# Kernel optimization log

Measured on AMD Instinct MI355X. Metric: run time of the kernel, lower is better.

The kernel has to match this reference:

```python
import jax, jax.numpy as jnp
import numpy as np

MIN_MAP = jnp.array([-3.602826, -3.602826, -3.602826], dtype=jnp.float32)

def _conv(x, w, stride, pad):
    return jax.lax.conv_general_dilated(x, w, (stride, stride), [(pad, pad), (pad, pad)],
                                        dimension_numbers=('NCHW', 'OIHW', 'NCHW'))

def _bn(x, g, b):
    # inference BatchNorm with running_mean=0, running_var=1 -> pure channel affine
    return x * g[None, :, None, None] + b[None, :, None, None]

def _maxpool2(x):
    return jax.lax.reduce_window(x, -jnp.inf, jax.lax.max, (1, 1, 2, 2), (1, 1, 2, 2), 'VALID')

def _rotations(angles):
    # angles: [N,3] (already multiplied by pi); matrix entries copied verbatim from the torch source
    c, s = jnp.cos(angles), jnp.sin(angles)
    z = jnp.zeros_like(c[:, 0]); o = jnp.ones_like(c[:, 0])
    Rx = jnp.stack([jnp.stack([o, z, z], -1),
                    jnp.stack([z, c[:, 0], s[:, 0]], -1),
                    jnp.stack([z, -s[:, 0], c[:, 0]], -1)], 1)
    Ry = jnp.stack([jnp.stack([c[:, 1], z, -s[:, 1]], -1),
                    jnp.stack([z, o, z], -1),
                    jnp.stack([s[:, 1], z, c[:, 1]], -1)], 1)
    Rz = jnp.stack([jnp.stack([c[:, 2], s[:, 2], z], -1),
                    jnp.stack([-s[:, 2], c[:, 2], z], -1),
                    jnp.stack([z, z, o], -1)], 1)
    return jnp.einsum('nij,njk,nkl->nil', Rx, Ry, Rz)  # [N,3,3]


def setup_inputs() -> dict:
    key = jax.random.key(0)
    ks = jax.random.split(key, 16)
    N, C, T, V, M = 32, 3, 224, 224, 2
    OC = 128
    def he(k, shape, fan_in):
        return jax.random.normal(k, shape, jnp.float32) * np.float32(np.sqrt(2.0 / fan_in))
    inp = {}
    inp['x'] = jax.random.normal(ks[0], (N, C, T, V, M), jnp.float32)
    inp['w1'] = he(ks[1], (OC, C, 5, 5), C * 25); inp['b1'] = jnp.zeros((OC,), jnp.float32)
    inp['g1'] = jnp.ones((OC,), jnp.float32); inp['be1'] = jnp.zeros((OC,), jnp.float32)
    inp['w2'] = he(ks[2], (OC, OC, 5, 5), OC * 25); inp['b2'] = jnp.zeros((OC,), jnp.float32)
    inp['g2'] = jnp.ones((OC,), jnp.float32); inp['be2'] = jnp.zeros((OC,), jnp.float32)
    feat = OC * (224 // 8) * (224 // 8)  # 100352
    inp['fw'] = jax.random.normal(ks[3], (6, feat), jnp.float32) * np.float32(np.sqrt(1.0 / feat))
    inp['fb'] = jnp.zeros((6,), jnp.float32)
    chans = [3, 64, 256, 512, 1024, 2048]  # surrogate ResNet-50-style /32 backbone
    for i in range(5):
        cin, cout = chans[i], chans[i + 1]
        inp['bw%d' % (i + 1)] = he(ks[4 + i], (cout, cin, 3, 3), cin * 9)
        inp['bg%d' % (i + 1)] = jnp.ones((cout,), jnp.float32)
        inp['bb%d' % (i + 1)] = jnp.zeros((cout,), jnp.float32)
    lin = 2048 * 7 * 7
    inp['lw'] = jax.random.normal(ks[10], (60, lin), jnp.float32) * np.float32(np.sqrt(1.0 / lin))
    inp['lb'] = jnp.zeros((60,), jnp.float32)
    return inp


def reference(x, w1, b1, g1, be1, w2, b2, g2, be2, fw, fb,
              bw1, bg1, bb1, bw2, bg2, bb2, bw3, bg3, bb3, bw4, bg4, bb4, bw5, bg5, bb5,
              lw, lb):
    N = x.shape[0]
    def person(xp):  # xp: [N,3,T,V]
        h = jax.nn.relu(_bn(_conv(xp, w1, 2, 2) + b1[None, :, None, None], g1, be1))
        h = jax.nn.relu(_bn(_conv(h, w2, 2, 2) + b2[None, :, None, None], g2, be2))
        h = _maxpool2(h)                       # [N,128,28,28]
        o = h.reshape(N, -1) @ fw.T + fb       # [N,6]
        # torch builds rotations from out[n,:3].item() -> constants w.r.t. autodiff
        R = _rotations(jax.lax.stop_gradient(o[:, :3]) * jnp.pi)
        xf = xp.reshape(N, 3, -1)
        rot = jnp.einsum('nij,njk->nik', R, xf)
        shift = jnp.einsum('nij,nj->ni', R, MIN_MAP[None, :] - o[:, 3:])
        bias = 255.0 * (shift - MIN_MAP[None, :]) / 8.812765
        z = (rot + bias[:, :, None]).reshape(xp.shape)
        for w, g, b in ((bw1, bg1, bb1), (bw2, bg2, bb2), (bw3, bg3, bb3),
                        (bw4, bg4, bb4), (bw5, bg5, bb5)):
            z = jax.nn.relu(_bn(_conv(z, w, 2, 1), g, b))
        return z  # [N,2048,7,7]
    out = jnp.maximum(person(x[..., 0]), person(x[..., 1]))
    return out.reshape(N, -1) @ lw.T + lb  # [N,60]
```

## Files before the change

### kernel.cpp

```cpp
#include <hip/hip_runtime.h>
#include <hip/hip_bf16.h>

typedef unsigned short u16;
typedef __attribute__((ext_vector_type(8))) short bf16x8;
typedef __attribute__((ext_vector_type(4))) float f32x4;
typedef __attribute__((ext_vector_type(8))) unsigned short u16x8;
typedef __attribute__((ext_vector_type(4))) unsigned short u16x4;

__device__ __forceinline__ u16 f2bf(float v) {
    __hip_bfloat16 b = __float2bfloat16(v);
    return *reinterpret_cast<u16*>(&b);
}
__device__ __forceinline__ float bf2f(u16 u) {
    __hip_bfloat16 b;
    *reinterpret_cast<u16*>(&b) = u;
    return __bfloat162float(b);
}

__device__ __forceinline__ void gl_lds16(const u16* g, u16* l) {
    __builtin_amdgcn_global_load_lds(
        (const __attribute__((address_space(1))) void*)g,
        (__attribute__((address_space(3))) void*)l, 16, 0, 0);
}

__global__ void repack_w32(const float* __restrict__ w, u16* __restrict__ wh,
                           int Cout, int Cin, int KK) {
    int i = blockIdx.x * blockDim.x + threadIdx.x;
    int tot = Cout * Cin * KK;
    if (i >= tot) return;
    int oc = i / (Cin * KK);
    int c = i - oc * (Cin * KK);
    int t = c >> 5, j = c & 31;
    int cs = t / KK, p = t - cs * KK;
    int ic = cs * 32 + j;
    wh[i] = f2bf(w[((size_t)oc * Cin + ic) * KK + p]);
}
__global__ void repack_split2(const float* __restrict__ w, u16* __restrict__ Ap,
                              int Cout, int CinR, int CinP, int KK, int Ksteps) {
    int cols = Ksteps * 64;
    int idx = blockIdx.x * blockDim.x + threadIdx.x;
    int tot = Cout * cols;
    if (idx >= tot) return;
    int oc = idx / cols, c = idx - oc * cols;
    int t = c >> 6, r = c & 63, half = r >> 5, j = r & 31;
    int cs = t / KK, p = t - cs * KK;
    int ic = cs * 32 + j;
    float v = (p < KK && ic < CinR) ? w[((size_t)oc * CinR + ic) * KK + p] : 0.f;
    u16 h = f2bf(v);
    Ap[idx] = half ? f2bf(v - bf2f(h)) : h;
}
__global__ void repack_g4_2(const float* __restrict__ w, u16* __restrict__ Ap,
                            int Cout, int CinR, int KS, int Ksteps) {
    int cols = Ksteps * 64;
    int idx = blockIdx.x * blockDim.x + threadIdx.x;
    int tot = Cout * cols;
    if (idx >= tot) return;
    int oc = idx / cols, c = idx - oc * cols;
    int t = c >> 6, r = c & 63, half = r >> 5, j = r & 31;
    int pix = j >> 2, ch = j & 3;
    float v = (pix < KS && ch < CinR)
                  ? w[(((size_t)oc * CinR + ch) * KS + t) * KS + pix] : 0.f;
    u16 h = f2bf(v);
    Ap[idx] = half ? f2bf(v - bf2f(h)) : h;
}
__global__ void repack_g4(const float* __restrict__ w, u16* __restrict__ Ap,
                          int Cout, int CinR, int KS, int Kpp) {
    int idx = blockIdx.x * blockDim.x + threadIdx.x;
    int tot = Cout * Kpp;
    if (idx >= tot) return;
    int oc = idx / Kpp, kk = idx - oc * Kpp;
    int ky = kk >> 5, r = kk & 31;
    int pix = r >> 2, ch = r & 3;
    float v = (pix < KS && ch < CinR)
                  ? w[(((size_t)oc * CinR + ch) * KS + ky) * KS + pix] : 0.f;
    Ap[idx] = f2bf(v);
}

__global__ void extract_person4(const float* __restrict__ x,
                                u16* __restrict__ X4, int m, int total) {
    int idx = blockIdx.x * blockDim.x + threadIdx.x;
    if (idx >= total) return;
    int n = idx / 50176;
    int p = idx - n * 50176;
    int y = p / 224, xx = p - y * 224;
    u16 h[4];
    h[3] = 0;
#pragma unroll
    for (int c = 0; c < 3; ++c)
        h[c] = f2bf(x[(((size_t)(n * 3 + c)) * 50176 + p) * 2 + m]);
    size_t o = (((size_t)n * 228 + y + 2) * 232 + xx + 2) * 4;
    *reinterpret_cast<u16x4*>(&X4[o]) = *reinterpret_cast<u16x4*>(h);
}

__global__ void zero_u16(u16* __restrict__ b, size_t n8) {
    size_t i = (size_t)blockIdx.x * blockDim.x + threadIdx.x;
    if (i >= n8) return;
    u16x8 z = {0, 0, 0, 0, 0, 0, 0, 0};
    *reinterpret_cast<u16x8*>(&b[i * 8]) = z;
}
__global__ void zero_halo(u16* __restrict__ buf, int Nn, int Hp, int Wp, int C,
                          int P, int H, int W) {
    int idx = blockIdx.x * blockDim.x + threadIdx.x;
    int tot = Nn * Hp * Wp;
    if (idx >= tot) return;
    int x = idx % Wp, t = idx / Wp, y = t % Hp;
    if (y >= P && y < P + H && x >= P && x < P + W) return;
    u16* p = buf + (size_t)idx * C;
    u16x8 z = {0, 0, 0, 0, 0, 0, 0, 0};
    for (int c = 0; c < C; c += 8) *reinterpret_cast<u16x8*>(&p[c]) = z;
}
__global__ void zero_halo_c4(u16* __restrict__ buf, int Nn, int Hp, int Wp,
                             int P, int H, int W) {
    int idx = blockIdx.x * blockDim.x + threadIdx.x;
    int tot = Nn * Hp * Wp;
    if (idx >= tot) return;
    int x = idx % Wp, t = idx / Wp, y = t % Hp;
    if (y >= P && y < P + H && x >= P && x < P + W) return;
    u16x4 z = {0, 0, 0, 0};
    *reinterpret_cast<u16x4*>(&buf[(size_t)idx * 4]) = z;
}

template <int BM, int CT, bool SPLIT, int MOUT>
__global__ __launch_bounds__(256) void gconv(
    const u16* __restrict__ A, const u16* __restrict__ B,
    const float* __restrict__ cbias, const float* __restrict__ gam,
    const float* __restrict__ bet,
    u16* __restrict__ outp, float* __restrict__ outf,
    int Nblk, int NHW, int Ksteps, int KSP,
    int Cin, int Hp_i, int Wp_i, int KS,
    int Wout, int HWout,
    int Cout, int Hp_o, int Wp_o, int P_o) {
    constexpr int WAVES_M = (BM == 128) ? 2 : 1;
    constexpr int WM = BM / WAVES_M;
    constexpr int WN = 128 / (4 / WAVES_M);
    constexpr int FM = WM / 16, FN = WN / 16;
    constexpr int ACOLS = SPLIT ? 64 : 32;
    constexpr int AR = (BM * ACOLS * 2) / 4096;

    __shared__ __align__(16) u16 Asb[2][BM * ACOLS];
    __shared__ __align__(16) u16 Bsb[2][128 * 32];

    const int tid = threadIdx.x;
    const int lane = tid & 63, wv = tid >> 6;

    const int nwg = gridDim.x, orig = blockIdx.x;
    const int qq = nwg >> 3, rr = nwg & 7, xcd = orig & 7;
    const int L = (xcd < rr ? xcd * (qq + 1) : rr * (qq + 1) + (xcd - rr) * qq) + (orig >> 3);
    const int gmK = nwg / Nblk;
    const int gm = gmK / KSP;
    const int bn = L / gmK;
    const int midK = L - bn * gmK;
    const int bm = midK % gm;
    const int kc = midK / gm;
    const int s0 = bn * 128, oc0 = bm * BM;

    const int nsteps = Ksteps;
    const int Arow = Ksteps * ACOLS;

    const u16* asrc[AR];
#pragma unroll
    for (int r = 0; r < AR; ++r) {
        int idx = r * 256 + tid;
        if constexpr (SPLIT) {
            int row = idx >> 3, slot = idx & 7;
            int c = slot ^ (row & 7);
            asrc[r] = A + (size_t)(oc0 + row) * Arow + c * 8;
        } else {
            int row = idx >> 2, slot = idx & 3;
            int q = slot ^ ((row >> 1) & 3);
            asrc[r] = A + (size_t)(oc0 + row) * Arow + q * 8;
        }
    }
    long brow[2];
#pragma unroll
    for (int r = 0; r < 2; ++r) {
        int idx = r * 256 + tid;
        int srow = idx >> 2;
        int q = (idx & 3) ^ ((idx >> 3) & 3);
        int s = s0 + srow;
        if (s > NHW - 1) s = NHW - 1;
        int n = s / HWout, pos = s - n * HWout;
        int oy = pos / Wout, ox = pos - oy * Wout;
        brow[r] = (((long)n * Hp_i + 2 * oy) * Wp_i + 2 * ox) * Cin + q * 8;
    }

    auto stage = [&](int buf, int t) {
        long ao = (long)t * ACOLS;
#pragma unroll
        for (int r = 0; r < AR; ++r)
            gl_lds16(asrc[r] + ao, &Asb[buf][(r * 256 + wv * 64) * 8]);
        long so;
        if constexpr (CT == 32) {
            int KK2 = KS * KS;
            int cs = t / KK2, p = t - cs * KK2;
            int ky = p / KS, kx = p - ky * KS;
            so = (long)(ky * Wp_i + kx) * Cin + cs * 32;
        } else {
            so = (long)t * Wp_i * 4;
        }
#pragma unroll
        for (int r = 0; r < 2; ++r)
            gl_lds16(B + brow[r] + so, &Bsb[buf][(r * 256 + wv * 64) * 8]);
    };

    const int cl = lane & 15, oct = lane >> 4;
    const int octx = oct ^ ((cl >> 1) & 3);
    const int aslot = oct ^ (cl & 7);
    const int wm0 = (WAVES_M == 2) ? (wv & 1) * WM : 0;
    const int wn0 = (WAVES_M == 2) ? (wv >> 1) * WN : wv * WN;

    f32x4 acc[FM][FN] = {};

    const int cs_steps = nsteps / KSP;
    const int t0 = kc * cs_steps, t1 = t0 + cs_steps;

    stage(0, t0);
    __syncthreads();
    for (int t = t0; t < t1; ++t) {
        const int cur = (t - t0) & 1;
        if (t + 1 < t1) stage(cur ^ 1, t + 1);
        bf16x8 af[FM], bfr[FN];
#pragma unroll
        for (int mi = 0; mi < FM; ++mi) {
            if constexpr (SPLIT)
                af[mi] = *reinterpret_cast<const bf16x8*>(
                    &Asb[cur][(wm0 + mi * 16 + cl) * ACOLS + aslot * 8]);
            else
                af[mi] = *reinterpret_cast<const bf16x8*>(
                    &Asb[cur][(wm0 + mi * 16 + cl) * ACOLS + octx * 8]);
        }
#pragma unroll
        for (int ni = 0; ni < FN; ++ni)
            bfr[ni] = *reinterpret_cast<const bf16x8*>(
                &Bsb[cur][(wn0 + ni * 16 + cl) * 32 + octx * 8]);
#pragma unroll
        for (int mi = 0; mi < FM; ++mi)
#pragma unroll
            for (int ni = 0; ni < FN; ++ni)
                acc[mi][ni] = __builtin_amdgcn_mfma_f32_16x16x32_bf16(
                    af[mi], bfr[ni], acc[mi][ni], 0, 0, 0);
        if constexpr (SPLIT) {
            bf16x8 al[FM];
#pragma unroll
            for (int mi = 0; mi < FM; ++mi)
                al[mi] = *reinterpret_cast<const bf16x8*>(
                    &Asb[cur][(wm0 + mi * 16 + cl) * ACOLS + (aslot ^ 4) * 8]);
#pragma unroll
            for (int mi = 0; mi < FM; ++mi)
#pragma unroll
                for (int ni = 0; ni < FN; ++ni)
                    acc[mi][ni] = __builtin_amdgcn_mfma_f32_16x16x32_bf16(
                        al[mi], bfr[ni], acc[mi][ni], 0, 0, 0);
        }
        __syncthreads();
    }

#pragma unroll
    for (int ni = 0; ni < FN; ++ni) {
        int s = s0 + wn0 + ni * 16 + cl;
        if (s >= NHW) continue;
        int n = s / HWout, pos = s - n * HWout;
        int oy = pos / Wout, ox = pos - oy * Wout;
#pragma unroll
        for (int mi = 0; mi < FM; ++mi) {
            int oc = oc0 + wm0 + mi * 16 + oct * 4;
            if constexpr (MOUT == 3) {
                float* pf = outf + (size_t)kc * ((size_t)NHW * Cout);
#pragma unroll
                for (int r3 = 0; r3 < 4; ++r3)
                    pf[((size_t)n * Cout + oc + r3) * HWout + pos] = acc[mi][ni][r3];
            } else if constexpr (MOUT == 2) {
#pragma unroll
                for (int r3 = 0; r3 < 4; ++r3) {
                    float v = acc[mi][ni][r3];
                    if (cbias) v += cbias[oc + r3];
                    v = fmaf(v, gam[oc + r3], bet[oc + r3]);
                    v = fmaxf(v, 0.f);
                    outf[((size_t)n * Cout + oc + r3) * HWout + pos] = v;
                }
            } else {
                u16 hh[4];
#pragma unroll
                for (int r3 = 0; r3 < 4; ++r3) {
                    float v = acc[mi][ni][r3];
                    if (cbias) v += cbias[oc + r3];
                    v = fmaf(v, gam[oc + r3], bet[oc + r3]);
                    v = fmaxf(v, 0.f);
                    hh[r3] = f2bf(v);
                }
                size_t ob = (((size_t)n * Hp_o + oy + P_o) * Wp_o + ox + P_o) * Cout + oc;
                *reinterpret_cast<u16x4*>(&outp[ob]) = *reinterpret_cast<u16x4*>(hh);
            }
        }
    }
}

__global__ void ksum_nchw(const float* __restrict__ part, const float* __restrict__ gam,
                          const float* __restrict__ bet, float* __restrict__ out,
                          size_t tot, size_t str, int HWout, int Cout, int KSP,
                          int domax) {
    size_t i = (size_t)blockIdx.x * blockDim.x + threadIdx.x;
    if (i >= tot) return;
    float s = 0.f;
    for (int kc = 0; kc < KSP; ++kc) s += part[kc * str + i];
    int oc = (int)((i / HWout) % Cout);
    float v = fmaxf(fmaf(s, gam[oc], bet[oc]), 0.f);
    out[i] = domax ? fmaxf(out[i], v) : v;
}
__global__ void ksum_nhwc(const float* __restrict__ part, const float* __restrict__ gam,
                          const float* __restrict__ bet, u16* __restrict__ outp,
                          int NHW, int HWout, int Wout, int Cout,
                          int Hp, int Wp, int P, int KSP, size_t str) {
    int ocq = Cout >> 2;
    int idx = blockIdx.x * blockDim.x + threadIdx.x;
    if (idx >= NHW * ocq) return;
    int s = idx / ocq;
    int oc = (idx - s * ocq) * 4;
    int n = s / HWout, pos = s - n * HWout;
    int oy = pos / Wout, ox = pos - oy * Wout;
    u16 hh[4];
#pragma unroll
    for (int j = 0; j < 4; ++j) {
        float v = 0.f;
        for (int kc = 0; kc < KSP; ++kc)
            v += part[kc * str + ((size_t)n * Cout + oc + j) * HWout + pos];
        v = fmaxf(fmaf(v, gam[oc + j], bet[oc + j]), 0.f);
        hh[j] = f2bf(v);
    }
    size_t ob = (((size_t)n * Hp + oy + P) * Wp + ox + P) * Cout + oc;
    *reinterpret_cast<u16x4*>(&outp[ob]) = *reinterpret_cast<u16x4*>(hh);
}

__global__ void maxpool2(const float* __restrict__ in, float* __restrict__ out,
                         int NC, int H, int W) {
    int Ho = H >> 1, Wo = W >> 1;
    size_t idx = (size_t)blockIdx.x * blockDim.x + threadIdx.x;
    size_t total = (size_t)NC * Ho * Wo;
    if (idx >= total) return;
    int ox = idx % Wo;
    size_t t = idx / Wo;
    int oy = t % Ho;
    int nc = t / Ho;
    const float* p = in + ((size_t)nc * H + oy * 2) * W + ox * 2;
    out[idx] = fmaxf(fmaxf(p[0], p[1]), fmaxf(p[W], p[W + 1]));
}

__global__ __launch_bounds__(256) void lin_part(
    const float* __restrict__ X, const float* __restrict__ W,
    float* __restrict__ partial, int K, int Kc, int Ncols, int Nn) {
    int c = blockIdx.x / Nn;
    int n = blockIdx.x - c * Nn;
    int lane = threadIdx.x & 63, wv = threadIdx.x >> 6;
    const float4* x4 = reinterpret_cast<const float4*>(X + (size_t)n * K + (size_t)c * Kc);
    int K4 = Kc >> 2;
    for (int j = wv; j < Ncols; j += 4) {
        const float4* w4 =
            reinterpret_cast<const float4*>(W + (size_t)j * K + (size_t)c * Kc);
        float s = 0.f;
        for (int k = lane; k < K4; k += 64) {
            float4 a = x4[k], b = w4[k];
            s = fmaf(a.x, b.x, s);
            s = fmaf(a.y, b.y, s);
            s = fmaf(a.z, b.z, s);
            s = fmaf(a.w, b.w, s);
        }
#pragma unroll
        for (int off = 32; off > 0; off >>= 1) s += __shfl_down(s, off, 64);
        if (lane == 0) partial[((size_t)c * Nn + n) * 64 + j] = s;
    }
}

__global__ void lin_reduce(const float* __restrict__ partial,
                           const float* __restrict__ bias, float* __restrict__ out,
                           int Ncols, int Nn, int nchunks) {
    int t = blockIdx.x * blockDim.x + threadIdx.x;
    if (t >= Nn * Ncols) return;
    int n = t / Ncols, j = t - n * Ncols;
    float s = bias[j];
    for (int c = 0; c < nchunks; ++c) s += partial[((size_t)c * Nn + n) * 64 + j];
    out[t] = s;
}

__global__ void make_rot(const float* __restrict__ o6, float* __restrict__ R,
                         float* __restrict__ bv, int Nc) {
    int n = threadIdx.x;
    if (n >= Nc) return;
    const float PI = 3.14159265358979323846f;
    float a0 = o6[n * 6 + 0] * PI, a1 = o6[n * 6 + 1] * PI, a2 = o6[n * 6 + 2] * PI;
    float c0 = cosf(a0), c1 = cosf(a1), c2 = cosf(a2);
    float s0 = sinf(a0), s1 = sinf(a1), s2 = sinf(a2);
    float Rx[9] = {1, 0, 0, 0, c0, s0, 0, -s0, c0};
    float Ry[9] = {c1, 0, -s1, 0, 1, 0, s1, 0, c1};
    float Rz[9] = {c2, s2, 0, -s2, c2, 0, 0, 0, 1};
    float M[9], Rm[9];
#pragma unroll
    for (int i = 0; i < 3; ++i)
#pragma unroll
        for (int j = 0; j < 3; ++j) {
            float acc = 0.f;
#pragma unroll
            for (int k = 0; k < 3; ++k) acc = fmaf(Ry[i * 3 + k], Rz[k * 3 + j], acc);
            M[i * 3 + j] = acc;
        }
#pragma unroll
    for (int i = 0; i < 3; ++i)
#pragma unroll
        for (int j = 0; j < 3; ++j) {
            float acc = 0.f;
#pragma unroll
            for (int k = 0; k < 3; ++k) acc = fmaf(Rx[i * 3 + k], M[k * 3 + j], acc);
            Rm[i * 3 + j] = acc;
        }
    const float MINV = -3.602826f;
    float v0 = MINV - o6[n * 6 + 3];
    float v1 = MINV - o6[n * 6 + 4];
    float v2 = MINV - o6[n * 6 + 5];
#pragma unroll
    for (int i = 0; i < 3; ++i) {
        float sh = Rm[i * 3 + 0] * v0 + Rm[i * 3 + 1] * v1 + Rm[i * 3 + 2] * v2;
        bv[n * 3 + i] = 255.f * (sh - MINV) / 8.812765f;
        R[n * 9 + i * 3 + 0] = Rm[i * 3 + 0];
        R[n * 9 + i * 3 + 1] = Rm[i * 3 + 1];
        R[n * 9 + i * 3 + 2] = Rm[i * 3 + 2];
    }
}

__global__ void rot_apply5(const float* __restrict__ xc, const float* __restrict__ R,
                           const float* __restrict__ bv, u16* __restrict__ z,
                           int m, int total) {
    int idx = blockIdx.x * blockDim.x + threadIdx.x;
    if (idx >= total) return;
    int n = idx / 50176;
    int p = idx - n * 50176;
    int y = p / 224, xx = p - y * 224;
    float x0 = xc[(((size_t)(n * 3 + 0)) * 50176 + p) * 2 + m];
    float x1 = xc[(((size_t)(n * 3 + 1)) * 50176 + p) * 2 + m];
    float x2 = xc[(((size_t)(n * 3 + 2)) * 50176 + p) * 2 + m];
    u16 o[4];
#pragma unroll
    for (int i = 0; i < 3; ++i) {
        float v = fmaf(R[n * 9 + i * 3 + 0], x0,
                  fmaf(R[n * 9 + i * 3 + 1], x1,
                  fmaf(R[n * 9 + i * 3 + 2], x2, bv[n * 3 + i])));
        o[i] = f2bf(v);
    }
    o[3] = 0;
    size_t ob = (((size_t)n * 226 + y + 1) * 232 + xx + 1) * 4;
    *reinterpret_cast<u16x4*>(&z[ob]) = *reinterpret_cast<u16x4*>(o);
}

static inline int nblk(size_t total, int bs) { return (int)((total + bs - 1) / bs); }

extern "C" void kernel_launch(void* const* d_in, const int* in_sizes, int n_in,
                              void* d_out, int out_size, void* d_ws, size_t ws_size,
                              hipStream_t stream) {
    const float* x   = (const float*)d_in[0];
    const float* w1  = (const float*)d_in[1];
    const float* b1  = (const float*)d_in[2];
    const float* g1  = (const float*)d_in[3];
    const float* be1 = (const float*)d_in[4];
    const float* w2  = (const float*)d_in[5];
    const float* b2  = (const float*)d_in[6];
    const float* g2  = (const float*)d_in[7];
    const float* be2 = (const float*)d_in[8];
    const float* fw  = (const float*)d_in[9];
    const float* fb  = (const float*)d_in[10];
    const float* bw[5], *bg[5], *bb[5];
    for (int i = 0; i < 5; ++i) {
        bw[i] = (const float*)d_in[11 + 3 * i];
        bg[i] = (const float*)d_in[12 + 3 * i];
        bb[i] = (const float*)d_in[13 + 3 * i];
    }
    const float* lw = (const float*)d_in[26];
    const float* lb = (const float*)d_in[27];
    float* out = (float*)d_out;

    const int N = 32;
    const int BS = 256;
    const size_t S_Pp = 100352;

    const size_t E_X4 = (size_t)228 * 232 * 4;
    const size_t E_B1 = (size_t)116 * 116 * 128;
    const size_t E_Zb2 = (size_t)114 * 114 * 64;
    const size_t E_Zb3 = (size_t)58 * 58 * 256;
    const size_t E_Zb4 = (size_t)30 * 30 * 512;
    const size_t E_Zb5 = (size_t)16 * 16 * 1024;

    const size_t slotC_B = E_Zb2 * 2;
    const size_t per_sample_B = E_X4 * 2 + E_B1 * 2 + slotC_B + S_Pp * 4;
    const size_t apack_u16 = (size_t)128 * 320 + (size_t)128 * 6400 + (size_t)64 * 96 +
                             (size_t)256 * 576 + (size_t)512 * 2304 +
                             (size_t)1024 * 4608 + (size_t)2048 * 9216;
    const size_t fixed_B = (size_t)N * S_Pp * 4 + 131072 * 4 + 8192 + apack_u16 * 2 + 4096;

    int Nc = N;
    while (Nc > 1 && (size_t)Nc * per_sample_B + fixed_B > ws_size) Nc >>= 1;

    char* cur = (char*)d_ws;
    auto alf = [&](size_t n) { float* p = (float*)cur; cur += ((n + 3) & ~(size_t)3) * 4; return p; };
    auto alu = [&](size_t n) { u16* p = (u16*)cur; cur += ((n + 7) & ~(size_t)7) * 2; return p; };

    float* PM = alf((size_t)N * S_Pp);
    float* O6 = alf(256);
    float* Rm = alf(384);
    float* BV = alf(384);
    float* LP = alf(131072);
    u16* Ap1 = alu((size_t)128 * 320);
    u16* Ap2 = alu((size_t)128 * 6400);
    u16* Ab1 = alu((size_t)64 * 96);
    u16* Ab2 = alu((size_t)256 * 576);
    u16* Ab3 = alu((size_t)512 * 2304);
    u16* Ab4 = alu((size_t)1024 * 4608);
    u16* Ab5 = alu((size_t)2048 * 9216);

    u16* X4p   = alu((size_t)Nc * E_X4);
    u16* Z16p  = X4p;
    u16* B1p   = alu((size_t)Nc * E_B1);
    u16* Zb3   = B1p;
    u16* Zb4   = Zb3 + (size_t)Nc * E_Zb3;
    u16* Zb5   = Zb4 + (size_t)Nc * E_Zb4;
    u16* SLOTC = alu((size_t)Nc * slotC_B / 2);
    float* C2f = (float*)SLOTC;
    u16* Zb2   = SLOTC;
    float* PartF = (float*)SLOTC;
    float* Pp  = alf((size_t)Nc * S_Pp);

    repack_g4_2<<<nblk((size_t)128 * 320, BS), BS, 0, stream>>>(w1, Ap1, 128, 3, 5, 5);
    repack_split2<<<nblk((size_t)128 * 6400, BS), BS, 0, stream>>>(w2, Ap2, 128, 128, 128, 25, 100);
    repack_g4<<<nblk((size_t)64 * 96, BS), BS, 0, stream>>>(bw[0], Ab1, 64, 3, 3, 96);
    repack_w32<<<nblk((size_t)256 * 576, BS), BS, 0, stream>>>(bw[1], Ab2, 256, 64, 9);
    repack_w32<<<nblk((size_t)512 * 2304, BS), BS, 0, stream>>>(bw[2], Ab3, 512, 256, 9);
    repack_w32<<<nblk((size_t)1024 * 4608, BS), BS, 0, stream>>>(bw[3], Ab4, 1024, 512, 9);
    repack_w32<<<nblk((size_t)2048 * 9216, BS), BS, 0, stream>>>(bw[4], Ab5, 2048, 1024, 9);

    zero_u16<<<nblk((size_t)Nc * E_X4 / 8, BS), BS, 0, stream>>>(X4p, (size_t)Nc * E_X4 / 8);

    const int NHW1 = Nc * 12544;
    const int Nb1 = (NHW1 + 127) / 128;
    const int NHW2 = Nc * 3136;
    const int Nb2 = (NHW2 + 127) / 128;
    const int NHW3 = Nc * 784;
    const int Nb3 = (NHW3 + 127) / 128;
    const int NHW4 = Nc * 196;
    const int Nb4 = (NHW4 + 127) / 128;
    const int NHW5 = Nc * 49;
    const int Nb5 = (NHW5 + 127) / 128;
    const size_t str4 = (size_t)NHW4 * 1024;
    const size_t str5 = (size_t)NHW5 * 2048;

    for (int m = 0; m < 2; ++m) {
        for (int c0 = 0; c0 < N; c0 += Nc) {
            const float* xc = x + (size_t)c0 * 150528 * 2;
            int nNP = Nc * 50176;
            zero_halo_c4<<<nblk((size_t)Nc * 228 * 232, BS), BS, 0, stream>>>(
                X4p, Nc, 228, 232, 2, 224, 224);
            extract_person4<<<nblk(nNP, BS), BS, 0, stream>>>(xc, X4p, m, nNP);

            zero_halo<<<nblk((size_t)Nc * 116 * 116, BS), BS, 0, stream>>>(B1p, Nc, 116, 116, 128, 2, 112, 112);

            gconv<128, 4, true, 0><<<Nb1, 256, 0, stream>>>(
                Ap1, X4p, b1, g1, be1, B1p, nullptr,
                Nb1, NHW1, 5, 1, 4, 228, 232, 5, 112, 12544, 128, 116, 116, 2);
            gconv<64, 32, true, 2><<<2 * Nb2, 256, 0, stream>>>(
                Ap2, B1p, b2, g2, be2, nullptr, C2f,
                Nb2, NHW2, 100, 1, 128, 116, 116, 5, 56, 3136, 128, 0, 0, 0);
            maxpool2<<<nblk((size_t)Nc * S_Pp, BS), BS, 0, stream>>>(C2f, Pp, Nc * 128, 56, 56);

            lin_part<<<64 * Nc, 256, 0, stream>>>(Pp, fw, LP, 100352, 1568, 6, Nc);
            lin_reduce<<<nblk(Nc * 6, 64), 64, 0, stream>>>(LP, fb, O6, 6, Nc, 64);
            make_rot<<<1, 64, 0, stream>>>(O6, Rm, BV, Nc);
            zero_halo_c4<<<nblk((size_t)Nc * 226 * 232, BS), BS, 0, stream>>>(
                Z16p, Nc, 226, 232, 1, 224, 224);
            rot_apply5<<<nblk(nNP, BS), BS, 0, stream>>>(xc, Rm, BV, Z16p, m, nNP);

            zero_halo<<<nblk((size_t)Nc * 114 * 114, BS), BS, 0, stream>>>(Zb2, Nc, 114, 114, 64, 1, 112, 112);
            zero_halo<<<nblk((size_t)Nc * 58 * 58, BS), BS, 0, stream>>>(Zb3, Nc, 58, 58, 256, 1, 56, 56);
            zero_halo<<<nblk((size_t)Nc * 30 * 30, BS), BS, 0, stream>>>(Zb4, Nc, 30, 30, 512, 1, 28, 28);
            zero_halo<<<nblk((size_t)Nc * 16 * 16, BS), BS, 0, stream>>>(Zb5, Nc, 16, 16, 1024, 1, 14, 14);

            gconv<64, 4, false, 0><<<Nb1, 256, 0, stream>>>(
                Ab1, Z16p, nullptr, bg[0], bb[0], Zb2, nullptr,
                Nb1, NHW1, 3, 1, 4, 226, 232, 3, 112, 12544, 64, 114, 114, 1);
            gconv<128, 32, false, 0><<<2 * Nb2, 256, 0, stream>>>(
                Ab2, Zb2, nullptr, bg[1], bb[1], Zb3, nullptr,
                Nb2, NHW2, 18, 1, 64, 114, 114, 3, 56, 3136, 256, 58, 58, 1);
            gconv<128, 32, false, 0><<<4 * Nb3, 256, 0, stream>>>(
                Ab3, Zb3, nullptr, bg[2], bb[2], Zb4, nullptr,
                Nb3, NHW3, 72, 1, 256, 58, 58, 3, 28, 784, 512, 30, 30, 1);
            gconv<128, 32, false, 3><<<8 * 2 * Nb4, 256, 0, stream>>>(
                Ab4, Zb4, nullptr, nullptr, nullptr, nullptr, PartF,
                Nb4, NHW4, 144, 2, 512, 30, 30, 3, 14, 196, 1024, 0, 0, 0);
            ksum_nhwc<<<nblk((size_t)NHW4 * 256, BS), BS, 0, stream>>>(
                PartF, bg[3], bb[3], Zb5, NHW4, 196, 14, 1024, 16, 16, 1, 2, str4);
            gconv<128, 32, false, 3><<<16 * 4 * Nb5, 256, 0, stream>>>(
                Ab5, Zb5, nullptr, nullptr, nullptr, nullptr, PartF,
                Nb5, NHW5, 288, 4, 1024, 16, 16, 3, 7, 49, 2048, 0, 0, 0);
            float* PMc = PM + (size_t)c0 * S_Pp;
            ksum_nchw<<<nblk((size_t)NHW5 * 2048, BS), BS, 0, stream>>>(
                PartF, bg[4], bb[4], PMc, (size_t)NHW5 * 2048, str5, 49, 2048, 4, m);
        }
    }

    lin_part<<<64 * N, 256, 0, stream>>>(PM, lw, LP, 100352, 1568, 60, N);
    lin_reduce<<<nblk(N * 60, 64), 64, 0, stream>>>(LP, lb, out, 60, N, 64);
}
```

Before: 1.988 ms.

## Store conv1 output as stride-2 parity planes for conv2 gathers

```diff
diff --git a/kernel.cpp b/kernel.cpp
--- a/kernel.cpp
+++ b/kernel.cpp
@@ -120,7 +120,7 @@
     *reinterpret_cast<u16x4*>(&buf[(size_t)idx * 4]) = z;
 }
 
-template <int BM, int CT, bool SPLIT, int MOUT>
+template <int BM, int CT, bool PAR, bool SPLIT, int MOUT>
 __global__ __launch_bounds__(256) void gconv(
     const u16* __restrict__ A, const u16* __restrict__ B,
     const float* __restrict__ cbias, const float* __restrict__ gam,
@@ -181,7 +181,10 @@
         if (s > NHW - 1) s = NHW - 1;
         int n = s / HWout, pos = s - n * HWout;
         int oy = pos / Wout, ox = pos - oy * Wout;
-        brow[r] = (((long)n * Hp_i + 2 * oy) * Wp_i + 2 * ox) * Cin + q * 8;
+        if constexpr (PAR)
+            brow[r] = ((long)(n * 58 + oy) * 58 + ox) * Cin + q * 8;
+        else
+            brow[r] = (((long)n * Hp_i + 2 * oy) * Wp_i + 2 * ox) * Cin + q * 8;
     }
 
     auto stage = [&](int buf, int t) {
@@ -194,7 +197,12 @@
             int KK2 = KS * KS;
             int cs = t / KK2, p = t - cs * KK2;
             int ky = p / KS, kx = p - ky * KS;
-            so = (long)(ky * Wp_i + kx) * Cin + cs * 32;
+            if constexpr (PAR) {
+                so = (long)((ky & 1) * 2 + (kx & 1)) * Hp_i * Cin +
+                     ((long)(ky >> 1) * 58 + (kx >> 1)) * Cin + cs * 32;
+            } else {
+                so = (long)(ky * Wp_i + kx) * Cin + cs * 32;
+            }
         } else {
             so = (long)t * Wp_i * 4;
         }
@@ -288,7 +296,14 @@
                     v = fmaxf(v, 0.f);
                     hh[r3] = f2bf(v);
                 }
-                size_t ob = (((size_t)n * Hp_o + oy + P_o) * Wp_o + ox + P_o) * Cout + oc;
+                size_t ob;
+                if constexpr (MOUT == 4) {
+                    ob = ((size_t)((oy & 1) * 2 + (ox & 1)) * Hp_o +
+                          ((size_t)n * 58 + ((oy + 2) >> 1)) * 58 +
+                          ((ox + 2) >> 1)) * Cout + oc;
+                } else {
+                    ob = (((size_t)n * Hp_o + oy + P_o) * Wp_o + ox + P_o) * Cout + oc;
+                }
                 *reinterpret_cast<u16x4*>(&outp[ob]) = *reinterpret_cast<u16x4*>(hh);
             }
         }
@@ -480,7 +495,7 @@
     const size_t S_Pp = 100352;
 
     const size_t E_X4 = (size_t)228 * 232 * 4;
-    const size_t E_B1 = (size_t)116 * 116 * 128;
+    const size_t E_B1 = (size_t)4 * 58 * 58 * 128;
     const size_t E_Zb2 = (size_t)114 * 114 * 64;
     const size_t E_Zb3 = (size_t)58 * 58 * 256;
     const size_t E_Zb4 = (size_t)30 * 30 * 512;
@@ -547,6 +562,7 @@
     const int Nb5 = (NHW5 + 127) / 128;
     const size_t str4 = (size_t)NHW4 * 1024;
     const size_t str5 = (size_t)NHW5 * 2048;
+    const int planePix = Nc * 58 * 58;
 
     for (int m = 0; m < 2; ++m) {
         for (int c0 = 0; c0 < N; c0 += Nc) {
@@ -556,14 +572,15 @@
                 X4p, Nc, 228, 232, 2, 224, 224);
             extract_person4<<<nblk(nNP, BS), BS, 0, stream>>>(xc, X4p, m, nNP);
 
-            zero_halo<<<nblk((size_t)Nc * 116 * 116, BS), BS, 0, stream>>>(B1p, Nc, 116, 116, 128, 2, 112, 112);
-
-            gconv<128, 4, true, 0><<<Nb1, 256, 0, stream>>>(
+            zero_halo<<<nblk((size_t)Nc * 4 * 58 * 58, BS), BS, 0, stream>>>(
+                B1p, Nc * 4, 58, 58, 128, 1, 56, 56);
+
+            gconv<128, 4, false, true, 4><<<Nb1, 256, 0, stream>>>(
                 Ap1, X4p, b1, g1, be1, B1p, nullptr,
-                Nb1, NHW1, 5, 1, 4, 228, 232, 5, 112, 12544, 128, 116, 116, 2);
-            gconv<64, 32, true, 2><<<2 * Nb2, 256, 0, stream>>>(
+                Nb1, NHW1, 5, 1, 4, 228, 232, 5, 112, 12544, 128, planePix, 0, 0);
+            gconv<64, 32, true, true, 2><<<2 * Nb2, 256, 0, stream>>>(
                 Ap2, B1p, b2, g2, be2, nullptr, C2f,
-                Nb2, NHW2, 100, 1, 128, 116, 116, 5, 56, 3136, 128, 0, 0, 0);
+                Nb2, NHW2, 100, 1, 128, planePix, 58, 5, 56, 3136, 128, 0, 0, 0);
             maxpool2<<<nblk((size_t)Nc * S_Pp, BS), BS, 0, stream>>>(C2f, Pp, Nc * 128, 56, 56);
 
             lin_part<<<64 * Nc, 256, 0, stream>>>(Pp, fw, LP, 100352, 1568, 6, Nc);
@@ -578,21 +595,21 @@
             zero_halo<<<nblk((size_t)Nc * 30 * 30, BS), BS, 0, stream>>>(Zb4, Nc, 30, 30, 512, 1, 28, 28);
             zero_halo<<<nblk((size_t)Nc * 16 * 16, BS), BS, 0, stream>>>(Zb5, Nc, 16, 16, 1024, 1, 14, 14);
 
-            gconv<64, 4, false, 0><<<Nb1, 256, 0, stream>>>(
+            gconv<64, 4, false, false, 0><<<Nb1, 256, 0, stream>>>(
                 Ab1, Z16p, nullptr, bg[0], bb[0], Zb2, nullptr,
                 Nb1, NHW1, 3, 1, 4, 226, 232, 3, 112, 12544, 64, 114, 114, 1);
-            gconv<128, 32, false, 0><<<2 * Nb2, 256, 0, stream>>>(
+            gconv<128, 32, false, false, 0><<<2 * Nb2, 256, 0, stream>>>(
                 Ab2, Zb2, nullptr, bg[1], bb[1], Zb3, nullptr,
                 Nb2, NHW2, 18, 1, 64, 114, 114, 3, 56, 3136, 256, 58, 58, 1);
-            gconv<128, 32, false, 0><<<4 * Nb3, 256, 0, stream>>>(
+            gconv<128, 32, false, false, 0><<<4 * Nb3, 256, 0, stream>>>(
                 Ab3, Zb3, nullptr, bg[2], bb[2], Zb4, nullptr,
                 Nb3, NHW3, 72, 1, 256, 58, 58, 3, 28, 784, 512, 30, 30, 1);
-            gconv<128, 32, false, 3><<<8 * 2 * Nb4, 256, 0, stream>>>(
+            gconv<128, 32, false, false, 3><<<8 * 2 * Nb4, 256, 0, stream>>>(
                 Ab4, Zb4, nullptr, nullptr, nullptr, nullptr, PartF,
                 Nb4, NHW4, 144, 2, 512, 30, 30, 3, 14, 196, 1024, 0, 0, 0);
             ksum_nhwc<<<nblk((size_t)NHW4 * 256, BS), BS, 0, stream>>>(
                 PartF, bg[3], bb[3], Zb5, NHW4, 196, 14, 1024, 16, 16, 1, 2, str4);
-            gconv<128, 32, false, 3><<<16 * 4 * Nb5, 256, 0, stream>>>(
+            gconv<128, 32, false, false, 3><<<16 * 4 * Nb5, 256, 0, stream>>>(
                 Ab5, Zb5, nullptr, nullptr, nullptr, nullptr, PartF,
                 Nb5, NHW5, 288, 4, 1024, 16, 16, 3, 7, 49, 2048, 0, 0, 0);
             float* PMc = PM + (size_t)c0 * S_Pp;
```

After: 2.009 ms. Within noise of the previous version (+1.0%).
